# Kernel optimization log

Hardware: AMD Instinct MI355X
Metric: run time of the kernel (lower is better)

The kernel has to match this reference:

```python
import jax, jax.numpy as jnp
import numpy as np

N_HEAD = 12
M_HIST = 5      # Anderson history window (AndersonAcceleration.m)
BETA = 1.0      # Anderson mixing (AndersonAcceleration.beta)
LN_EPS = 1e-5


def _layer_norm(x, w, b):
    mu = x.mean(-1, keepdims=True)
    xc = x - mu
    var = (xc * xc).mean(-1, keepdims=True)
    return xc * jax.lax.rsqrt(var + LN_EPS) * w + b


def _mha(x, wqkv, bqkv, wo, bo):
    # torch nn.MultiheadAttention, batch_first, self-attention, no mask, dropout=0
    B, T, C = x.shape
    dh = C // N_HEAD
    qkv = x @ wqkv.T + bqkv                       # [B,T,3C]
    q, k, v = jnp.split(qkv, 3, axis=-1)
    def heads(t):
        return t.reshape(B, T, N_HEAD, dh).transpose(0, 2, 1, 3)  # [B,H,T,dh]
    q, k, v = heads(q), heads(k), heads(v)
    scores = jnp.einsum('bhqd,bhkd->bhqk', q, k) / jnp.sqrt(jnp.asarray(dh, x.dtype))
    att = jax.nn.softmax(scores, axis=-1)
    out = jnp.einsum('bhqk,bhkd->bhqd', att, v).transpose(0, 2, 1, 3).reshape(B, T, C)
    return out @ wo.T + bo


def _deq_delta(z, u, emb_row, ln1_w, ln1_b, in_proj_w, in_proj_b, out_proj_w,
               out_proj_b, ln2_w, ln2_b, mlp_w1, mlp_b1, mlp_w2, mlp_b2):
    # DEQOperator.forward -> delta_z
    z_temporal = z + 0.1 * emb_row                 # broadcast [C] over [B,T,C]
    z_ctx = z_temporal + u
    x = _layer_norm(z_ctx, ln1_w, ln1_b)
    attn_out = _mha(x, in_proj_w, in_proj_b, out_proj_w, out_proj_b)
    z_attn = z + attn_out
    h = _layer_norm(z_attn, ln2_w, ln2_b)
    h = jax.nn.gelu(h @ mlp_w1.T + mlp_b1, approximate=False) @ mlp_w2.T + mlp_b2
    z_mlp = z_attn + h
    return z_mlp - z


def _deq_solve(u, iter_emb, ln1_w, ln1_b, in_proj_w, in_proj_b, out_proj_w,
               out_proj_b, ln2_w, ln2_b, mlp_w1, mlp_b1, mlp_w2, mlp_b2, num_iters):
    B, T, C = u.shape
    z = jnp.zeros_like(u)
    Xs, Fs = [], []   # Anderson history of states / residuals
    max_row = iter_emb.shape[0] - 1
    for it in range(num_iters):
        emb_row = iter_emb[min(it, max_row)]
        delta = _deq_delta(z, u, emb_row, ln1_w, ln1_b, in_proj_w, in_proj_b,
                           out_proj_w, out_proj_b, ln2_w, ln2_b,
                           mlp_w1, mlp_b1, mlp_w2, mlp_b2)
        res = delta  # residual of f(z) = z + delta_z w.r.t. z
        Xs.append(z); Fs.append(res)
        if len(Xs) > M_HIST:
            Xs.pop(0); Fs.pop(0)
        if len(Xs) == 1:
            z = z + BETA * res
        else:
            K = len(Xs) - 1
            dF = jnp.stack(Fs[:-1], 0) - res[None]               # [K,B,T,C]
            dF_f = dF.transpose(1, 2, 0, 3).reshape(B * T, K, C)  # per-token LS
            r_f = res.reshape(B * T, C)
            G = jnp.einsum('nkc,nlc->nkl', dF_f, dF_f)            # [BT,K,K]
            G = G + 1e-6 * jnp.eye(K, dtype=u.dtype)
            bvec = jnp.einsum('nkc,nc->nk', dF_f, r_f)            # [BT,K]
            alpha = jnp.linalg.solve(G, bvec[..., None])[..., 0]
            d = r_f - jnp.einsum('nkc,nk->nc', dF_f, alpha)
            z = (z.reshape(B * T, C) + BETA * d).reshape(B, T, C)
    return z


def setup_inputs() -> dict:
    key = jax.random.key(0)
    ks = jax.random.split(key, 6)
    B, T, C = 4, 1024, 768
    std = 0.02
    return {
        'u': jax.random.normal(ks[0], (B, T, C), jnp.float32),
        'iter_emb': std * jax.random.normal(ks[1], (31, C), jnp.float32),
        'ln1_w': jnp.ones((C,), jnp.float32),
        'ln1_b': jnp.zeros((C,), jnp.float32),
        'in_proj_w': std * jax.random.normal(ks[2], (3 * C, C), jnp.float32),
        'in_proj_b': jnp.zeros((3 * C,), jnp.float32),
        'out_proj_w': std * jax.random.normal(ks[3], (C, C), jnp.float32),
        'out_proj_b': jnp.zeros((C,), jnp.float32),
        'ln2_w': jnp.ones((C,), jnp.float32),
        'ln2_b': jnp.zeros((C,), jnp.float32),
        'mlp_w1': std * jax.random.normal(ks[4], (4 * C, C), jnp.float32),
        'mlp_b1': jnp.zeros((4 * C,), jnp.float32),
        'mlp_w2': std * jax.random.normal(ks[5], (C, 4 * C), jnp.float32),
        'mlp_b2': jnp.zeros((C,), jnp.float32),
        'num_iters': 6,
    }


def reference(u, iter_emb, ln1_w, ln1_b, in_proj_w, in_proj_b, out_proj_w,
              out_proj_b, ln2_w, ln2_b, mlp_w1, mlp_b1, mlp_w2, mlp_b2, num_iters):
    return _deq_solve(u, iter_emb, ln1_w, ln1_b, in_proj_w, in_proj_b,
                      out_proj_w, out_proj_b, ln2_w, ln2_b,
                      mlp_w1, mlp_b1, mlp_w2, mlp_b2, int(num_iters))
```

## Files before the change

### kernel.cpp

```cpp
#include <hip/hip_runtime.h>
#include <math.h>

#define BT 4096
#define CDIM 768
#define NHEAD 12
#define DH 64
#define TSEQ 1024
#define BBATCH 4

typedef _Float16 f16;
typedef __attribute__((ext_vector_type(4))) _Float16 f16x4;
typedef __attribute__((ext_vector_type(8))) _Float16 f16x8;
typedef __attribute__((ext_vector_type(4))) float f32x4;

typedef const __attribute__((address_space(1))) unsigned int* gas1_t;
typedef __attribute__((address_space(3))) unsigned int* las3_t;
__device__ __forceinline__ void glds16(const void* g, void* l) {
  __builtin_amdgcn_global_load_lds((gas1_t)g, (las3_t)l, 16, 0, 0);
}

__device__ __forceinline__ float block_reduce_sum(float v, float* sbuf) {
#pragma unroll
  for (int o = 32; o > 0; o >>= 1) v += __shfl_down(v, o, 64);
  int lane = threadIdx.x & 63;
  int w = threadIdx.x >> 6;
  if (lane == 0) sbuf[w] = v;
  __syncthreads();
  float r = sbuf[0] + sbuf[1] + sbuf[2] + sbuf[3];
  __syncthreads();
  return r;
}

__global__ __launch_bounds__(256) void zero_kernel(float4* __restrict__ p) {
  p[(size_t)blockIdx.x * 256 + threadIdx.x] = make_float4(0.f, 0.f, 0.f, 0.f);
}

__global__ __launch_bounds__(256) void cvt_f16_kernel(
    const float* __restrict__ in, f16* __restrict__ out) {
  size_t i = ((size_t)blockIdx.x * 256 + threadIdx.x) * 4;
  float4 v = *(const float4*)(in + i);
  f16x4 o = {(f16)v.x, (f16)v.y, (f16)v.z, (f16)v.w};
  *(f16x4*)(out + i) = o;
}

__global__ __launch_bounds__(256) void ln1_kernel(
    const float* __restrict__ z, const float* __restrict__ u,
    const float* __restrict__ emb, const float* __restrict__ w,
    const float* __restrict__ b, f16* __restrict__ x) {
  __shared__ float sbuf[4];
  int row = blockIdx.x;
  int tid = threadIdx.x;
  const float* zr = z + (size_t)row * CDIM;
  const float* ur = u + (size_t)row * CDIM;
  float v[3];
  float s = 0.f;
#pragma unroll
  for (int i = 0; i < 3; i++) {
    int c = tid + i * 256;
    v[i] = zr[c] + 0.1f * emb[c] + ur[c];
    s += v[i];
  }
  s = block_reduce_sum(s, sbuf);
  float mu = s * (1.f / CDIM);
  float sq = 0.f;
#pragma unroll
  for (int i = 0; i < 3; i++) { v[i] -= mu; sq += v[i] * v[i]; }
  sq = block_reduce_sum(sq, sbuf);
  float rstd = rsqrtf(sq * (1.f / CDIM) + 1e-5f);
  f16* xr = x + (size_t)row * CDIM;
#pragma unroll
  for (int i = 0; i < 3; i++) {
    int c = tid + i * 256;
    xr[c] = (f16)(v[i] * rstd * w[c] + b[c]);
  }
}

__global__ __launch_bounds__(256) void ln2_kernel(
    const float* __restrict__ in, const float* __restrict__ w,
    const float* __restrict__ b, f16* __restrict__ x,
    const float* __restrict__ z, const float* __restrict__ b2,
    float* __restrict__ rinit) {
  __shared__ float sbuf[4];
  int row = blockIdx.x;
  int tid = threadIdx.x;
  const float* ir = in + (size_t)row * CDIM;
  const float* zr = z + (size_t)row * CDIM;
  float* rr = rinit + (size_t)row * CDIM;
  float v[3];
  float s = 0.f;
#pragma unroll
  for (int i = 0; i < 3; i++) {
    int c = tid + i * 256;
    v[i] = ir[c];
    rr[c] = v[i] - zr[c] + b2[c];
    s += v[i];
  }
  s = block_reduce_sum(s, sbuf);
  float mu = s * (1.f / CDIM);
  float sq = 0.f;
#pragma unroll
  for (int i = 0; i < 3; i++) { v[i] -= mu; sq += v[i] * v[i]; }
  sq = block_reduce_sum(sq, sbuf);
  float rstd = rsqrtf(sq * (1.f / CDIM) + 1e-5f);
  f16* xr = x + (size_t)row * CDIM;
#pragma unroll
  for (int i = 0; i < 3; i++) {
    int c = tid + i * 256;
    xr[c] = (f16)(v[i] * rstd * w[c] + b[c]);
  }
}

__device__ __forceinline__ float gelu_exact(float t) {
  return 0.5f * t * (1.f + erff(t * 0.70710678118654752f));
}

template <int MODE>
__global__ __launch_bounds__(256, 3) void gemm_mfma(
    const f16* __restrict__ A, const f16* __restrict__ W,
    const float* __restrict__ bias, f16* __restrict__ hq,
    f16* __restrict__ hk, f16* __restrict__ hvt, f16* __restrict__ hout,
    int M, int N, int K) {
  __shared__ __align__(16) f16 As[128 * 64];
  __shared__ __align__(16) f16 Bs[128 * 64];
  int tid = threadIdx.x;
  int wv = tid >> 6, lane = tid & 63;
  int bm = blockIdx.y, bn = blockIdx.x;
  int wm = (wv >> 1) * 64, wn = (wv & 1) * 64;

  int srow = wv * 32 + (lane >> 3);
  int scole = 8 * ((lane & 7) ^ (lane >> 3));
  const f16* gA = A + (size_t)(bm * 128 + srow) * K + scole;
  const f16* gB = W + (size_t)(bn * 128 + srow) * K + scole;

  f32x4 acc[4][4];
#pragma unroll
  for (int i = 0; i < 4; i++)
#pragma unroll
    for (int j = 0; j < 4; j++) acc[i][j] = (f32x4){0.f, 0.f, 0.f, 0.f};

  int am = lane & 15;
  int quad = lane >> 4;
  int sx = am & 7;

  for (int k0 = 0; k0 < K; k0 += 64) {
    __syncthreads();
#pragma unroll
    for (int j = 0; j < 4; j++) {
      glds16(gA + (size_t)(j * 8) * K + k0, &As[(wv * 32 + j * 8) * 64]);
      glds16(gB + (size_t)(j * 8) * K + k0, &Bs[(wv * 32 + j * 8) * 64]);
    }
    __syncthreads();
#pragma unroll
    for (int kk = 0; kk < 2; kk++) {
      int ce = 8 * (((kk << 2) + quad) ^ sx);
      f16x8 af[4], bfr[4];
#pragma unroll
      for (int mi = 0; mi < 4; mi++)
        af[mi] = *(const f16x8*)&As[(wm + mi * 16 + am) * 64 + ce];
#pragma unroll
      for (int nj = 0; nj < 4; nj++)
        bfr[nj] = *(const f16x8*)&Bs[(wn + nj * 16 + am) * 64 + ce];
#pragma unroll
      for (int mi = 0; mi < 4; mi++)
#pragma unroll
        for (int nj = 0; nj < 4; nj++)
          acc[mi][nj] = __builtin_amdgcn_mfma_f32_16x16x32_f16(
              af[mi], bfr[nj], acc[mi][nj], 0, 0, 0);
    }
  }

  int crow0 = bm * 128 + wm + quad * 4;
  int ccol0 = bn * 128 + wn + am;
#pragma unroll
  for (int nj = 0; nj < 4; nj++) {
    int col = ccol0 + nj * 16;
    float bcol = bias[col];
    if constexpr (MODE == 3) {
      int which = col / CDIM;
      int rem = col - which * CDIM;
      int h = rem >> 6;
      int d = rem & 63;
#pragma unroll
      for (int mi = 0; mi < 4; mi++) {
#pragma unroll
        for (int r = 0; r < 4; r++) {
          int m = crow0 + mi * 16 + r;
          int bb = m >> 10, t = m & 1023;
          f16 val = (f16)(acc[mi][nj][r] + bcol);
          if (which == 0)
            hq[(((size_t)(bb * NHEAD + h) * TSEQ + t) << 6) + d] = val;
          else if (which == 1)
            hk[(((size_t)(bb * NHEAD + h) * TSEQ + t) << 6) + d] = val;
          else
            hvt[(((size_t)(bb * NHEAD + h) * DH + d) << 10) + t] = val;
        }
      }
    } else {
#pragma unroll
      for (int mi = 0; mi < 4; mi++) {
#pragma unroll
        for (int r = 0; r < 4; r++) {
          int m = crow0 + mi * 16 + r;
          size_t idx = (size_t)m * N + col;
          hout[idx] = (f16)gelu_exact(acc[mi][nj][r] + bcol);
        }
      }
    }
  }
}

template <int MODE>
__global__ __launch_bounds__(256, 6) void gemm_glds64(
    const f16* __restrict__ A, const f16* __restrict__ W,
    const float* __restrict__ bias, const float* __restrict__ aux1,
    float* __restrict__ fout0, int M, int N, int K) {
  __shared__ __align__(16) f16 As[64 * 64];
  __shared__ __align__(16) f16 Bs[64 * 64];
  int tid = threadIdx.x;
  int wv = tid >> 6, lane = tid & 63;
  int bm = blockIdx.x, bn = blockIdx.y;
  int wm = (wv >> 1) * 32, wn = (wv & 1) * 32;

  int ks = (MODE == 4) ? blockIdx.z : 0;
  int kl = (MODE == 4) ? (K >> 1) : K;

  int srow = wv * 16 + (lane >> 3);
  int scole = 8 * ((lane & 7) ^ (lane >> 3));
  const f16* gA = A + (size_t)(bm * 64 + srow) * K + ks * kl + scole;
  const f16* gB = W + (size_t)(bn * 64 + srow) * K + ks * kl + scole;

  f32x4 acc[2][2];
#pragma unroll
  for (int i = 0; i < 2; i++)
#pragma unroll
    for (int j = 0; j < 2; j++) acc[i][j] = (f32x4){0.f, 0.f, 0.f, 0.f};

  int am = lane & 15;
  int quad = lane >> 4;
  int sx = am & 7;

  for (int k0 = 0; k0 < kl; k0 += 64) {
    __syncthreads();
#pragma unroll
    for (int j = 0; j < 2; j++) {
      glds16(gA + (size_t)(j * 8) * K + k0, &As[(wv * 16 + j * 8) * 64]);
      glds16(gB + (size_t)(j * 8) * K + k0, &Bs[(wv * 16 + j * 8) * 64]);
    }
    __syncthreads();
#pragma unroll
    for (int kk = 0; kk < 2; kk++) {
      int ce = 8 * (((kk << 2) + quad) ^ sx);
      f16x8 af[2], bfr[2];
#pragma unroll
      for (int mi = 0; mi < 2; mi++)
        af[mi] = *(const f16x8*)&As[(wm + mi * 16 + am) * 64 + ce];
#pragma unroll
      for (int nj = 0; nj < 2; nj++)
        bfr[nj] = *(const f16x8*)&Bs[(wn + nj * 16 + am) * 64 + ce];
#pragma unroll
      for (int mi = 0; mi < 2; mi++)
#pragma unroll
        for (int nj = 0; nj < 2; nj++)
          acc[mi][nj] = __builtin_amdgcn_mfma_f32_16x16x32_f16(
              af[mi], bfr[nj], acc[mi][nj], 0, 0, 0);
    }
  }

  int crow0 = bm * 64 + wm + quad * 4;
  int ccol0 = bn * 64 + wn + am;
#pragma unroll
  for (int nj = 0; nj < 2; nj++) {
    int col = ccol0 + nj * 16;
#pragma unroll
    for (int mi = 0; mi < 2; mi++) {
#pragma unroll
      for (int r = 0; r < 4; r++) {
        int m = crow0 + mi * 16 + r;
        size_t idx = (size_t)m * N + col;
        if constexpr (MODE == 0) {
          fout0[idx] = acc[mi][nj][r] + bias[col] + aux1[idx];
        } else {
          unsafeAtomicAdd(fout0 + idx, acc[mi][nj][r]);
        }
      }
    }
  }
}

#define PSTRIDE 72
#define KVS 72
__global__ __launch_bounds__(256, 3) void flash_attn8(
    const f16* __restrict__ Qg, const f16* __restrict__ Kg,
    const f16* __restrict__ Vt, f16* __restrict__ attn) {
  __shared__ __align__(16) f16 Ks[64 * KVS];
  __shared__ __align__(16) f16 Vs[64 * KVS];
  __shared__ __align__(16) f16 Plds[4][16 * PSTRIDE];
  int tid = threadIdx.x;
  int wv = tid >> 6, lane = tid & 63;
  int bh = blockIdx.x;
  int bb = bh / NHEAD, h = bh % NHEAD;
  int m0 = (blockIdx.y * 4 + wv) * 16;
  int am = lane & 15;
  int quad = lane >> 4;
  int ak = quad * 8;

  int srow = tid >> 3;
  int scol = (tid & 7) * 8;

  const f16* kb = Kg + (((size_t)bh * TSEQ) << 6);
  const f16* vb = Vt + (((size_t)bh * DH) << 10);

  const f16* qbase = Qg + (((size_t)bh * TSEQ + m0) << 6);
  f16x8 qf0 = *(const f16x8*)(qbase + am * 64 + ak);
  f16x8 qf1 = *(const f16x8*)(qbase + am * 64 + 32 + ak);
#pragma unroll
  for (int i = 0; i < 8; i++) { qf0[i] *= (f16)0.125f; qf1[i] *= (f16)0.125f; }

  f16* Pw = Plds[wv];
  f32x4 Oa[4];
#pragma unroll
  for (int i = 0; i < 4; i++) Oa[i] = (f32x4){0.f, 0.f, 0.f, 0.f};
  float lpart[4] = {0.f, 0.f, 0.f, 0.f};

  f16x8 kr0 = *(const f16x8*)(kb + (size_t)srow * 64 + scol);
  f16x8 kr1 = *(const f16x8*)(kb + (size_t)(32 + srow) * 64 + scol);
  f16x8 vr0 = *(const f16x8*)(vb + (size_t)srow * TSEQ + scol);
  f16x8 vr1 = *(const f16x8*)(vb + (size_t)(32 + srow) * TSEQ + scol);

  for (int n0 = 0; n0 < TSEQ; n0 += 64) {
    __syncthreads();
    *(f16x8*)&Ks[srow * KVS + scol] = kr0;
    *(f16x8*)&Ks[(32 + srow) * KVS + scol] = kr1;
    *(f16x8*)&Vs[srow * KVS + scol] = vr0;
    *(f16x8*)&Vs[(32 + srow) * KVS + scol] = vr1;
    __syncthreads();
    int nn = n0 + 64;
    if (nn < TSEQ) {
      kr0 = *(const f16x8*)(kb + (size_t)(nn + srow) * 64 + scol);
      kr1 = *(const f16x8*)(kb + (size_t)(nn + 32 + srow) * 64 + scol);
      vr0 = *(const f16x8*)(vb + (size_t)srow * TSEQ + nn + scol);
      vr1 = *(const f16x8*)(vb + (size_t)(32 + srow) * TSEQ + nn + scol);
    }
    f32x4 S[4];
#pragma unroll
    for (int t = 0; t < 4; t++) {
      f16x8 kf0 = *(const f16x8*)&Ks[(16 * t + am) * KVS + ak];
      f16x8 kf1 = *(const f16x8*)&Ks[(16 * t + am) * KVS + 32 + ak];
      S[t] = __builtin_amdgcn_mfma_f32_16x16x32_f16(
          qf0, kf0, (f32x4){0.f, 0.f, 0.f, 0.f}, 0, 0, 0);
      S[t] = __builtin_amdgcn_mfma_f32_16x16x32_f16(qf1, kf1, S[t], 0, 0, 0);
    }
#pragma unroll
    for (int t = 0; t < 4; t++) {
#pragma unroll
      for (int r = 0; r < 4; r++) {
        float p = __expf(S[t][r]);
        lpart[r] += p;
        Pw[(quad * 4 + r) * PSTRIDE + 16 * t + am] = (f16)p;
      }
    }
    f16x8 pa0 = *(const f16x8*)&Pw[am * PSTRIDE + ak];
    f16x8 pa1 = *(const f16x8*)&Pw[am * PSTRIDE + 32 + ak];
#pragma unroll
    for (int dt = 0; dt < 4; dt++) {
      f16x8 vf0 = *(const f16x8*)&Vs[(16 * dt + am) * KVS + ak];
      f16x8 vf1 = *(const f16x8*)&Vs[(16 * dt + am) * KVS + 32 + ak];
      Oa[dt] = __builtin_amdgcn_mfma_f32_16x16x32_f16(pa0, vf0, Oa[dt], 0, 0, 0);
      Oa[dt] = __builtin_amdgcn_mfma_f32_16x16x32_f16(pa1, vf1, Oa[dt], 0, 0, 0);
    }
  }

#pragma unroll
  for (int o = 1; o < 16; o <<= 1)
#pragma unroll
    for (int r = 0; r < 4; r++) lpart[r] += __shfl_xor(lpart[r], o, 64);

#pragma unroll
  for (int r = 0; r < 4; r++) {
    int m = m0 + quad * 4 + r;
    float inv = 1.f / lpart[r];
    f16* orow = attn + ((size_t)(bb * TSEQ + m)) * CDIM + h * DH;
#pragma unroll
    for (int dt = 0; dt < 4; dt++)
      orow[dt * 16 + am] = (f16)(Oa[dt][r] * inv);
  }
}

template <int KA>
__global__ __launch_bounds__(256) void anderson_ln1(
    float* __restrict__ z, const float* __restrict__ rescur,
    const float* __restrict__ p0, const float* __restrict__ p1,
    const float* __restrict__ p2, const float* __restrict__ p3,
    const float* __restrict__ u, const float* __restrict__ emb,
    const float* __restrict__ w, const float* __restrict__ b,
    f16* __restrict__ x) {
  __shared__ float sbuf[4];
  int row = blockIdx.x, tid = threadIdx.x;
  size_t base = (size_t)row * CDIM + tid;
  float r[3];
#pragma unroll
  for (int i = 0; i < 3; i++) r[i] = rescur[base + i * 256];

  float zn[3];
  if constexpr (KA == 0) {
#pragma unroll
    for (int i = 0; i < 3; i++) zn[i] = z[base + i * 256] + r[i];
  } else {
    const float* ps[4] = {p0, p1, p2, p3};
    float dF[KA == 0 ? 1 : KA][3];
#pragma unroll
    for (int k = 0; k < KA; k++)
#pragma unroll
      for (int i = 0; i < 3; i++) dF[k][i] = ps[k][base + i * 256] - r[i];

    float Gm[KA == 0 ? 1 : KA][KA == 0 ? 1 : KA], bv[KA == 0 ? 1 : KA];
#pragma unroll
    for (int k = 0; k < KA; k++) {
#pragma unroll
      for (int ll = k; ll < KA; ll++) {
        float p = 0.f;
#pragma unroll
        for (int i = 0; i < 3; i++) p += dF[k][i] * dF[ll][i];
        float t = block_reduce_sum(p, sbuf);
        Gm[k][ll] = t;
        Gm[ll][k] = t;
      }
    }
#pragma unroll
    for (int k = 0; k < KA; k++) Gm[k][k] += 1e-6f;
#pragma unroll
    for (int k = 0; k < KA; k++) {
      float p = 0.f;
#pragma unroll
      for (int i = 0; i < 3; i++) p += dF[k][i] * r[i];
      bv[k] = block_reduce_sum(p, sbuf);
    }
    float alpha[KA == 0 ? 1 : KA];
#pragma unroll
    for (int p = 0; p < KA; p++) {
      float inv = 1.f / Gm[p][p];
#pragma unroll
      for (int rr = p + 1; rr < KA; rr++) {
        float f = Gm[rr][p] * inv;
#pragma unroll
        for (int c = p; c < KA; c++) Gm[rr][c] -= f * Gm[p][c];
        bv[rr] -= f * bv[p];
      }
    }
#pragma unroll
    for (int p = KA - 1; p >= 0; p--) {
      float s2 = bv[p];
#pragma unroll
      for (int c = p + 1; c < KA; c++) s2 -= Gm[p][c] * alpha[c];
      alpha[p] = s2 / Gm[p][p];
    }
#pragma unroll
    for (int i = 0; i < 3; i++) {
      float d = r[i];
#pragma unroll
      for (int k = 0; k < KA; k++) d = fmaf(-dF[k][i], alpha[k], d);
      zn[i] = z[base + i * 256] + d;
    }
  }
#pragma unroll
  for (int i = 0; i < 3; i++) z[base + i * 256] = zn[i];

  const float* ur = u + (size_t)row * CDIM;
  float v[3];
  float s = 0.f;
#pragma unroll
  for (int i = 0; i < 3; i++) {
    int c = tid + i * 256;
    v[i] = zn[i] + 0.1f * emb[c] + ur[c];
    s += v[i];
  }
  s = block_reduce_sum(s, sbuf);
  float mu = s * (1.f / CDIM);
  float sq = 0.f;
#pragma unroll
  for (int i = 0; i < 3; i++) { v[i] -= mu; sq += v[i] * v[i]; }
  sq = block_reduce_sum(sq, sbuf);
  float rstd = rsqrtf(sq * (1.f / CDIM) + 1e-5f);
  f16* xr = x + (size_t)row * CDIM;
#pragma unroll
  for (int i = 0; i < 3; i++) {
    int c = tid + i * 256;
    xr[c] = (f16)(v[i] * rstd * w[c] + b[c]);
  }
}

template <int KA>
__global__ __launch_bounds__(256) void anderson_kernel(
    float* __restrict__ z, const float* __restrict__ rescur,
    const float* __restrict__ p0, const float* __restrict__ p1,
    const float* __restrict__ p2, const float* __restrict__ p3) {
  __shared__ float sbuf[4];
  int row = blockIdx.x, tid = threadIdx.x;
  size_t base = (size_t)row * CDIM + tid;
  float r[3];
#pragma unroll
  for (int i = 0; i < 3; i++) r[i] = rescur[base + i * 256];
  const float* ps[4] = {p0, p1, p2, p3};
  float dF[KA][3];
#pragma unroll
  for (int k = 0; k < KA; k++)
#pragma unroll
    for (int i = 0; i < 3; i++) dF[k][i] = ps[k][base + i * 256] - r[i];

  float Gm[KA][KA], bv[KA];
#pragma unroll
  for (int k = 0; k < KA; k++) {
#pragma unroll
    for (int ll = k; ll < KA; ll++) {
      float p = 0.f;
#pragma unroll
      for (int i = 0; i < 3; i++) p += dF[k][i] * dF[ll][i];
      float t = block_reduce_sum(p, sbuf);
      Gm[k][ll] = t;
      Gm[ll][k] = t;
    }
  }
#pragma unroll
  for (int k = 0; k < KA; k++) Gm[k][k] += 1e-6f;
#pragma unroll
  for (int k = 0; k < KA; k++) {
    float p = 0.f;
#pragma unroll
    for (int i = 0; i < 3; i++) p += dF[k][i] * r[i];
    bv[k] = block_reduce_sum(p, sbuf);
  }
  float alpha[KA];
#pragma unroll
  for (int p = 0; p < KA; p++) {
    float inv = 1.f / Gm[p][p];
#pragma unroll
    for (int rr = p + 1; rr < KA; rr++) {
      float f = Gm[rr][p] * inv;
#pragma unroll
      for (int c = p; c < KA; c++) Gm[rr][c] -= f * Gm[p][c];
      bv[rr] -= f * bv[p];
    }
  }
#pragma unroll
  for (int p = KA - 1; p >= 0; p--) {
    float s2 = bv[p];
#pragma unroll
    for (int c = p + 1; c < KA; c++) s2 -= Gm[p][c] * alpha[c];
    alpha[p] = s2 / Gm[p][p];
  }
#pragma unroll
  for (int i = 0; i < 3; i++) {
    float d = r[i];
#pragma unroll
    for (int k = 0; k < KA; k++) d = fmaf(-dF[k][i], alpha[k], d);
    z[base + i * 256] += d;
  }
}

extern "C" void kernel_launch(void* const* d_in, const int* in_sizes, int n_in,
                              void* d_out, int out_size, void* d_ws,
                              size_t ws_size, hipStream_t stream) {
  (void)in_sizes; (void)n_in; (void)out_size; (void)ws_size;
  const float* u = (const float*)d_in[0];
  const float* iter_emb = (const float*)d_in[1];
  const float* ln1w = (const float*)d_in[2];
  const float* ln1b = (const float*)d_in[3];
  const float* wqkv = (const float*)d_in[4];
  const float* bqkv = (const float*)d_in[5];
  const float* wo = (const float*)d_in[6];
  const float* bo = (const float*)d_in[7];
  const float* ln2w = (const float*)d_in[8];
  const float* ln2b = (const float*)d_in[9];
  const float* w1 = (const float*)d_in[10];
  const float* b1 = (const float*)d_in[11];
  const float* w2 = (const float*)d_in[12];
  const float* b2 = (const float*)d_in[13];

  const size_t S = (size_t)BT * CDIM;
  float* ws = (float*)d_ws;
  float* z = ws + 0 * S;
  float* zattn = ws + 1 * S;
  float* res[5] = {ws + 2 * S, ws + 3 * S, ws + 4 * S, ws + 5 * S, ws + 6 * S};
  f16* q_h = (f16*)(ws + 7 * S);
  f16* k_h = q_h + S;
  f16* vt_h = q_h + 2 * S;
  f16* h_h = (f16*)(ws + 7 * S);
  f16* x_h = (f16*)(ws + 9 * S);
  f16* wqkv_h = x_h + S;
  f16* wo_h = wqkv_h + (size_t)3 * CDIM * CDIM;
  f16* w1_h = wo_h + (size_t)CDIM * CDIM;
  f16* w2_h = w1_h + (size_t)4 * CDIM * CDIM;

  cvt_f16_kernel<<<1728, 256, 0, stream>>>(wqkv, wqkv_h);
  cvt_f16_kernel<<<576, 256, 0, stream>>>(wo, wo_h);
  cvt_f16_kernel<<<2304, 256, 0, stream>>>(w1, w1_h);
  cvt_f16_kernel<<<2304, 256, 0, stream>>>(w2, w2_h);
  zero_kernel<<<S / 1024, 256, 0, stream>>>((float4*)z);

  for (int it = 0; it < 6; it++) {
    float* rcur = res[it % 5];
    if (it == 0) {
      ln1_kernel<<<BT, 256, 0, stream>>>(z, u, iter_emb, ln1w, ln1b, x_h);
    }
    gemm_mfma<3><<<dim3(18, 32), 256, 0, stream>>>(
        x_h, wqkv_h, bqkv, q_h, k_h, vt_h, nullptr, BT, 3 * CDIM, CDIM);
    flash_attn8<<<dim3(BBATCH * NHEAD, TSEQ / 64), 256, 0, stream>>>(
        q_h, k_h, vt_h, x_h);
    gemm_glds64<0><<<dim3(64, 12), 256, 0, stream>>>(
        x_h, wo_h, bo, z, zattn, BT, CDIM, CDIM);
    ln2_kernel<<<BT, 256, 0, stream>>>(zattn, ln2w, ln2b, x_h, z, b2, rcur);
    gemm_mfma<1><<<dim3(24, 32), 256, 0, stream>>>(
        x_h, w1_h, b1, nullptr, nullptr, nullptr, h_h, BT, 4 * CDIM, CDIM);
    gemm_glds64<4><<<dim3(64, 12, 2), 256, 0, stream>>>(
        h_h, w2_h, b2, nullptr, rcur, BT, CDIM, 4 * CDIM);

    int Kh = it < 4 ? it : 4;
    const float* p[4] = {rcur, rcur, rcur, rcur};
    for (int kx = 1; kx <= Kh; kx++) p[kx - 1] = res[(it - kx) % 5];
    if (it < 5) {
      const float* embn = iter_emb + (it + 1) * CDIM;
      switch (Kh) {
        case 0: anderson_ln1<0><<<BT, 256, 0, stream>>>(z, rcur, p[0], p[1], p[2], p[3], u, embn, ln1w, ln1b, x_h); break;
        case 1: anderson_ln1<1><<<BT, 256, 0, stream>>>(z, rcur, p[0], p[1], p[2], p[3], u, embn, ln1w, ln1b, x_h); break;
        case 2: anderson_ln1<2><<<BT, 256, 0, stream>>>(z, rcur, p[0], p[1], p[2], p[3], u, embn, ln1w, ln1b, x_h); break;
        case 3: anderson_ln1<3><<<BT, 256, 0, stream>>>(z, rcur, p[0], p[1], p[2], p[3], u, embn, ln1w, ln1b, x_h); break;
        default: anderson_ln1<4><<<BT, 256, 0, stream>>>(z, rcur, p[0], p[1], p[2], p[3], u, embn, ln1w, ln1b, x_h); break;
      }
    } else {
      anderson_kernel<4><<<BT, 256, 0, stream>>>(z, rcur, p[0], p[1], p[2], p[3]);
    }
  }
  hipMemcpyAsync(d_out, z, S * sizeof(float), hipMemcpyDeviceToDevice, stream);
}
```

Before: 1.182 ms.

## Use tanh-approx GELU and double-buffer LDS in small-tile GEMM

Replaces the exact erf-based GELU in the MLP up-projection epilogue with a tanh-form approximation written as a sigmoid via __expf, which cuts transcendental cost but no longer matches the reference's exact GELU. Separately, the 64x64 global-to-LDS GEMM is double-buffered: the next K tile is loaded into a second LDS buffer while the current one feeds MFMAs, with one barrier per iteration instead of two. The extra LDS lowers the occupancy hint from 6 to 4 blocks per CU.

```diff
diff --git a/kernel.cpp b/kernel.cpp
--- a/kernel.cpp
+++ b/kernel.cpp
@@ -110,8 +110,11 @@
   }
 }
 
-__device__ __forceinline__ float gelu_exact(float t) {
-  return 0.5f * t * (1.f + erff(t * 0.70710678118654752f));
+__device__ __forceinline__ float gelu_fast(float t) {
+  float a = 1.5957691f * (t + 0.044715f * t * t * t);
+  a = fminf(fmaxf(a, -30.f), 30.f);
+  float e = __expf(a);
+  return t * e / (e + 1.f);
 }
 
 template <int MODE>
@@ -202,7 +205,7 @@
         for (int r = 0; r < 4; r++) {
           int m = crow0 + mi * 16 + r;
           size_t idx = (size_t)m * N + col;
-          hout[idx] = (f16)gelu_exact(acc[mi][nj][r] + bcol);
+          hout[idx] = (f16)gelu_fast(acc[mi][nj][r] + bcol);
         }
       }
     }
@@ -210,12 +213,12 @@
 }
 
 template <int MODE>
-__global__ __launch_bounds__(256, 6) void gemm_glds64(
+__global__ __launch_bounds__(256, 4) void gemm_glds64(
     const f16* __restrict__ A, const f16* __restrict__ W,
     const float* __restrict__ bias, const float* __restrict__ aux1,
     float* __restrict__ fout0, int M, int N, int K) {
-  __shared__ __align__(16) f16 As[64 * 64];
-  __shared__ __align__(16) f16 Bs[64 * 64];
+  __shared__ __align__(16) f16 As[2][64 * 64];
+  __shared__ __align__(16) f16 Bs[2][64 * 64];
   int tid = threadIdx.x;
   int wv = tid >> 6, lane = tid & 63;
   int bm = blockIdx.x, bn = blockIdx.y;
@@ -239,24 +242,35 @@
   int quad = lane >> 4;
   int sx = am & 7;
 
+#pragma unroll
+  for (int j = 0; j < 2; j++) {
+    glds16(gA + (size_t)(j * 8) * K, &As[0][(wv * 16 + j * 8) * 64]);
+    glds16(gB + (size_t)(j * 8) * K, &Bs[0][(wv * 16 + j * 8) * 64]);
+  }
+  __syncthreads();
+
+  int cur = 0;
   for (int k0 = 0; k0 < kl; k0 += 64) {
-    __syncthreads();
-#pragma unroll
-    for (int j = 0; j < 2; j++) {
-      glds16(gA + (size_t)(j * 8) * K + k0, &As[(wv * 16 + j * 8) * 64]);
-      glds16(gB + (size_t)(j * 8) * K + k0, &Bs[(wv * 16 + j * 8) * 64]);
-    }
-    __syncthreads();
+    int kn = k0 + 64;
+    if (kn < kl) {
+#pragma unroll
+      for (int j = 0; j < 2; j++) {
+        glds16(gA + (size_t)(j * 8) * K + kn,
+               &As[cur ^ 1][(wv * 16 + j * 8) * 64]);
+        glds16(gB + (size_t)(j * 8) * K + kn,
+               &Bs[cur ^ 1][(wv * 16 + j * 8) * 64]);
+      }
+    }
 #pragma unroll
     for (int kk = 0; kk < 2; kk++) {
       int ce = 8 * (((kk << 2) + quad) ^ sx);
       f16x8 af[2], bfr[2];
 #pragma unroll
       for (int mi = 0; mi < 2; mi++)
-        af[mi] = *(const f16x8*)&As[(wm + mi * 16 + am) * 64 + ce];
+        af[mi] = *(const f16x8*)&As[cur][(wm + mi * 16 + am) * 64 + ce];
 #pragma unroll
       for (int nj = 0; nj < 2; nj++)
-        bfr[nj] = *(const f16x8*)&Bs[(wn + nj * 16 + am) * 64 + ce];
+        bfr[nj] = *(const f16x8*)&Bs[cur][(wn + nj * 16 + am) * 64 + ce];
 #pragma unroll
       for (int mi = 0; mi < 2; mi++)
 #pragma unroll
@@ -264,6 +278,8 @@
           acc[mi][nj] = __builtin_amdgcn_mfma_f32_16x16x32_f16(
               af[mi], bfr[nj], acc[mi][nj], 0, 0, 0);
     }
+    __syncthreads();
+    cur ^= 1;
   }
 
   int crow0 = bm * 64 + wm + quad * 4;
```

New measurement: 1.176 ms. Within noise of the previous version (-0.6%).
